# Performance work log

Measured on AMD Instinct MI355X. Metric: run time of the kernel, lower is better.

The kernel has to match this reference:

```python
import jax, jax.numpy as jnp
import numpy as np

DIM = 128
HEADS = 4
WS = 7          # window_size
N = WS * WS     # tokens per window
B_ = 4096       # total windows (64 images x 64 windows)
NW = 64         # windows per image (mask groups)


def _rel_position_index():
    # Matches the torch buffer construction exactly (static, int).
    coords = np.stack(np.meshgrid(np.arange(WS), np.arange(WS), indexing='ij'))
    coords_flat = coords.reshape(2, -1)                      # [2, N]
    rel = coords_flat[:, :, None] - coords_flat[:, None, :]  # [2, N, N]
    rel = rel.transpose(1, 2, 0).copy()                      # [N, N, 2]
    rel[:, :, 0] += WS - 1
    rel[:, :, 1] += WS - 1
    rel[:, :, 0] *= 2 * WS - 1
    return jnp.asarray(rel.sum(-1))                          # [N, N] int


REL_INDEX = _rel_position_index()


def setup_inputs() -> dict:
    key = jax.random.key(0)
    ks = jax.random.split(key, 7)
    x = jax.random.normal(ks[0], (B_, N, DIM), dtype=jnp.float32)
    # shift-style additive mask per window group: mostly 0, some -100
    mask = jnp.where(jax.random.uniform(ks[1], (NW, N, N)) < 0.1, -100.0, 0.0).astype(jnp.float32)
    qkv_w = jax.random.normal(ks[2], (3 * DIM, DIM), dtype=jnp.float32) * (DIM ** -0.5)
    qkv_b = jnp.zeros((3 * DIM,), dtype=jnp.float32)
    proj_w = jax.random.normal(ks[3], (DIM, DIM), dtype=jnp.float32) * (DIM ** -0.5)
    proj_b = jnp.zeros((DIM,), dtype=jnp.float32)
    bias_table = jax.random.normal(ks[4], ((2 * WS - 1) ** 2, HEADS), dtype=jnp.float32) * 0.02
    return {"x": x, "mask": mask, "qkv_w": qkv_w, "qkv_b": qkv_b,
            "proj_w": proj_w, "proj_b": proj_b, "bias_table": bias_table}


def reference(x, mask, qkv_w, qkv_b, proj_w, proj_b, bias_table):
    Bw, Nn, C = x.shape
    H = HEADS
    hd = C // H
    scale = hd ** -0.5
    qkv = (x @ qkv_w.T + qkv_b).reshape(Bw, Nn, 3, H, hd)
    q = jnp.moveaxis(qkv[:, :, 0], 2, 1)  # [B_, H, N, hd]
    k = jnp.moveaxis(qkv[:, :, 1], 2, 1)
    v = jnp.moveaxis(qkv[:, :, 2], 2, 1)
    attn = jnp.einsum('bhnd,bhmd->bhnm', q * scale, k)        # [B_, H, N, N]
    bias = bias_table[REL_INDEX].transpose(2, 0, 1)            # [H, N, N]
    attn = attn + bias[None]
    nW = mask.shape[0]
    attn = attn.reshape(Bw // nW, nW, H, Nn, Nn) + mask[None, :, None]
    attn = attn.reshape(Bw, H, Nn, Nn)
    attn = jax.nn.softmax(attn, axis=-1)
    out = jnp.einsum('bhnm,bhmd->bhnd', attn, v)               # [B_, H, N, hd]
    out = out.transpose(0, 2, 1, 3).reshape(Bw, Nn, C)
    return out @ proj_w.T + proj_b
```

## Files before the change

### kernel.cpp

```cpp
#include <hip/hip_runtime.h>
#include <stdint.h>

typedef float  f32x4   __attribute__((ext_vector_type(4)));
typedef float  float4v __attribute__((ext_vector_type(4)));
typedef short  short4v __attribute__((ext_vector_type(4)));
typedef short  short8v __attribute__((ext_vector_type(8)));
typedef __bf16 bf16x8  __attribute__((ext_vector_type(8)));

static __device__ __forceinline__ short f2bf(float f) {
  unsigned u = __builtin_bit_cast(unsigned, f);
  u += 0x7FFFu + ((u >> 16) & 1u);
  return (short)(u >> 16);
}

static __device__ __forceinline__ f32x4 mfma16(short8v a, short8v b, f32x4 c) {
  return __builtin_amdgcn_mfma_f32_16x16x32_bf16(
      __builtin_bit_cast(bf16x8, a), __builtin_bit_cast(bf16x8, b), c, 0, 0, 0);
}

static __device__ __forceinline__ short8v cat44(short4v a, short4v b) {
  short8v r;
  r[0] = a[0]; r[1] = a[1]; r[2] = a[2]; r[3] = a[3];
  r[4] = b[0]; r[5] = b[1]; r[6] = b[2]; r[7] = b[3];
  return r;
}

__global__ void cvt_weights_kernel(const float* __restrict__ qkv_w,
                                   const float* __restrict__ proj_w,
                                   short* __restrict__ wq, short* __restrict__ wp) {
  int i = blockIdx.x * 256 + threadIdx.x;
  wq[i] = f2bf(qkv_w[i]);
  if (i < 16384) wp[i] = f2bf(proj_w[i]);
}

__global__ void build_cmb_kernel(const float* __restrict__ mask,
                                 const float* __restrict__ bias_table,
                                 float* __restrict__ cmb) {
  int id   = blockIdx.x * 256 + threadIdx.x;
  int lane = id & 63;
  int i    = (id >> 6) & 3;
  int qt   = (id >> 8) & 3;
  int h    = (id >> 10) & 3;
  int w    = id >> 12;
  int q     = qt * 16 + (lane & 15);
  int kbase = i * 16 + ((lane >> 4) << 2);
  f32x4 v;
#pragma unroll
  for (int r = 0; r < 4; ++r) {
    int key = kbase + r;
    float val;
    if (key >= 49) {
      val = -1e30f;
    } else if (q >= 49) {
      val = 0.f;
    } else {
      int qi = q / 7, qj = q - qi * 7;
      int ki = key / 7, kj = key - ki * 7;
      int ridx = (qi - ki + 6) * 13 + (qj - kj + 6);
      val = bias_table[ridx * 4 + h] + mask[w * 2401 + q * 49 + key];
    }
    v[r] = val;
  }
  ((f32x4*)cmb)[id] = v;
}

__global__ __launch_bounds__(256, 2)
void win_attn_kernel(const float* __restrict__ x,
                     const float* __restrict__ qkv_b,
                     const float* __restrict__ proj_b,
                     const short* __restrict__ wq,
                     const short* __restrict__ wp,
                     const float* __restrict__ cmb,
                     float* __restrict__ out) {
  __shared__ __align__(16) short smem[17408];
  short* xb  = smem;
  short* vtm = smem + 8704;
  short* aom = smem;

  const int b    = blockIdx.x;
  const int tid  = threadIdx.x;
  const int lane = tid & 63;
  const int h    = tid >> 6;
  const int l15  = lane & 15;
  const int lhi  = lane >> 4;
  const int cb   = lhi * 8;

  {
    short4v z = {0, 0, 0, 0};
    for (int idx = tid; idx < 510; idx += 256)
      *(short4v*)&xb[49 * 136 + idx * 4] = z;
    const float* xw = x + (long)b * (49 * 128);
    for (int idx = tid; idx < 1568; idx += 256) {
      int m  = idx >> 5;
      int c0 = (idx & 31) << 2;
      float4v v = *(const float4v*)&xw[m * 128 + c0];
      short4v s;
      s[0] = f2bf(v[0]); s[1] = f2bf(v[1]); s[2] = f2bf(v[2]); s[3] = f2bf(v[3]);
      *(short4v*)&xb[m * 136 + c0] = s;
    }
  }
  __syncthreads();

  short8v qfr[4], kfr[4];
  {
    f32x4 qa[2][4], ka[2][4];
#pragma unroll
    for (int nt = 0; nt < 2; ++nt) {
      const f32x4 bq4 = *(const f32x4*)&qkv_b[h * 32 + nt * 16 + lhi * 4];
      const f32x4 bk4 = *(const f32x4*)&qkv_b[128 + h * 32 + nt * 16 + lhi * 4];
#pragma unroll
      for (int jt = 0; jt < 4; ++jt) { qa[nt][jt] = bq4; ka[nt][jt] = bk4; }
    }
#pragma unroll
    for (int ks = 0; ks < 4; ++ks) {
      short8v a[4];
#pragma unroll
      for (int jt = 0; jt < 4; ++jt)
        a[jt] = *(const short8v*)&xb[(jt * 16 + l15) * 136 + ks * 32 + cb];
#pragma unroll
      for (int nt = 0; nt < 2; ++nt) {
        const short8v bq =
            *(const short8v*)&wq[(h * 32 + nt * 16 + l15) * 128 + ks * 32 + cb];
        const short8v bk =
            *(const short8v*)&wq[(128 + h * 32 + nt * 16 + l15) * 128 + ks * 32 + cb];
#pragma unroll
        for (int jt = 0; jt < 4; ++jt) {
          qa[nt][jt] = mfma16(bq, a[jt], qa[nt][jt]);
          ka[nt][jt] = mfma16(bk, a[jt], ka[nt][jt]);
        }
      }
    }
    const float scale = 0.1767766952966369f;
#pragma unroll
    for (int jt = 0; jt < 4; ++jt) {
      short8v qv, kv;
#pragma unroll
      for (int nt = 0; nt < 2; ++nt)
#pragma unroll
        for (int r = 0; r < 4; ++r) {
          qv[nt * 4 + r] = f2bf(qa[nt][jt][r] * scale);
          kv[nt * 4 + r] = f2bf(ka[nt][jt][r]);
        }
      qfr[jt] = qv;
      kfr[jt] = kv;
    }
  }

  {
    f32x4 va[2][4];
#pragma unroll
    for (int nt = 0; nt < 2; ++nt) {
      const float vb = qkv_b[256 + h * 32 + nt * 16 + l15];
#pragma unroll
      for (int mt = 0; mt < 4; ++mt) va[nt][mt] = f32x4{vb, vb, vb, vb};
    }
#pragma unroll
    for (int ks = 0; ks < 4; ++ks) {
      short8v a[4];
#pragma unroll
      for (int mt = 0; mt < 4; ++mt)
        a[mt] = *(const short8v*)&xb[(mt * 16 + l15) * 136 + ks * 32 + cb];
#pragma unroll
      for (int nt = 0; nt < 2; ++nt) {
        const short8v bv =
            *(const short8v*)&wq[(256 + h * 32 + nt * 16 + l15) * 128 + ks * 32 + cb];
#pragma unroll
        for (int mt = 0; mt < 4; ++mt)
          va[nt][mt] = mfma16(a[mt], bv, va[nt][mt]);
      }
    }
#pragma unroll
    for (int nt = 0; nt < 2; ++nt)
#pragma unroll
      for (int mt = 0; mt < 4; ++mt) {
        short4v p;
#pragma unroll
        for (int r = 0; r < 4; ++r) p[r] = f2bf(va[nt][mt][r]);
        *(short4v*)&vtm[h * 2176 + (nt * 16 + l15) * 68 + mt * 16 + lhi * 4] = p;
      }
  }

  f32x4 o[2][4];
#pragma unroll
  for (int dt = 0; dt < 2; ++dt)
#pragma unroll
    for (int jt = 0; jt < 4; ++jt) o[dt][jt] = f32x4{0.f, 0.f, 0.f, 0.f};
  {
    const f32x4* cmb4 = (const f32x4*)cmb;
    const long cbase = (long)(b & 63) * 4096 + h * 1024 + lane;

#pragma unroll
    for (int jt = 0; jt < 4; ++jt) {
      f32x4 s[4];
#pragma unroll
      for (int i = 0; i < 4; ++i)
        s[i] = mfma16(kfr[i], qfr[jt], cmb4[cbase + jt * 256 + i * 64]);

      float mx = s[0][0];
#pragma unroll
      for (int i = 0; i < 4; ++i)
#pragma unroll
        for (int r = 0; r < 4; ++r) mx = fmaxf(mx, s[i][r]);
      mx = fmaxf(mx, __shfl_xor(mx, 16));
      mx = fmaxf(mx, __shfl_xor(mx, 32));
      float sum = 0.f;
#pragma unroll
      for (int i = 0; i < 4; ++i)
#pragma unroll
        for (int r = 0; r < 4; ++r) {
          float e = __expf(s[i][r] - mx);
          s[i][r] = e;
          sum += e;
        }
      sum += __shfl_xor(sum, 16);
      sum += __shfl_xor(sum, 32);
      const float inv = 1.f / sum;

      short8v pb[2];
#pragma unroll
      for (int ks = 0; ks < 2; ++ks) {
        short8v pv;
#pragma unroll
        for (int e = 0; e < 4; ++e) pv[e]     = f2bf(s[2 * ks][e] * inv);
#pragma unroll
        for (int e = 0; e < 4; ++e) pv[4 + e] = f2bf(s[2 * ks + 1][e] * inv);
        pb[ks] = pv;
      }

#pragma unroll
      for (int dt = 0; dt < 2; ++dt)
#pragma unroll
        for (int ks = 0; ks < 2; ++ks) {
          const int va = h * 2176 + (dt * 16 + l15) * 68 + ks * 32 + lhi * 4;
          short8v vfr = cat44(*(const short4v*)&vtm[va], *(const short4v*)&vtm[va + 16]);
          o[dt][jt] = mfma16(vfr, pb[ks], o[dt][jt]);
        }
    }
  }
  __syncthreads();

#pragma unroll
  for (int dt = 0; dt < 2; ++dt)
#pragma unroll
    for (int jt = 0; jt < 4; ++jt) {
      short4v p;
#pragma unroll
      for (int r = 0; r < 4; ++r) p[r] = f2bf(o[dt][jt][r]);
      *(short4v*)&aom[(jt * 16 + l15) * 136 + h * 32 + dt * 16 + lhi * 4] = p;
    }
  __syncthreads();

  {
    f32x4 po[2][4];
#pragma unroll
    for (int nt = 0; nt < 2; ++nt) {
      const float pbv = proj_b[h * 32 + nt * 16 + l15];
#pragma unroll
      for (int mt = 0; mt < 4; ++mt) po[nt][mt] = f32x4{pbv, pbv, pbv, pbv};
    }
#pragma unroll
    for (int ks = 0; ks < 4; ++ks) {
      short8v p[4];
#pragma unroll
      for (int mt = 0; mt < 4; ++mt)
        p[mt] = *(const short8v*)&aom[(mt * 16 + l15) * 136 + ks * 32 + cb];
#pragma unroll
      for (int nt = 0; nt < 2; ++nt) {
        const short8v wfr =
            *(const short8v*)&wp[(h * 32 + nt * 16 + l15) * 128 + ks * 32 + cb];
#pragma unroll
        for (int mt = 0; mt < 4; ++mt)
          po[nt][mt] = mfma16(p[mt], wfr, po[nt][mt]);
      }
    }
    float* outw = out + (long)b * (49 * 128);
#pragma unroll
    for (int nt = 0; nt < 2; ++nt) {
      const int ncol = h * 32 + nt * 16 + l15;
#pragma unroll
      for (int mt = 0; mt < 4; ++mt)
#pragma unroll
        for (int r = 0; r < 4; ++r) {
          const int m0 = mt * 16 + lhi * 4 + r;
          if (m0 < 49) outw[m0 * 128 + ncol] = po[nt][mt][r];
        }
    }
  }
}

extern "C" void kernel_launch(void* const* d_in, const int* in_sizes, int n_in,
                              void* d_out, int out_size, void* d_ws, size_t ws_size,
                              hipStream_t stream) {
  const float* x          = (const float*)d_in[0];
  const float* mask       = (const float*)d_in[1];
  const float* qkv_w      = (const float*)d_in[2];
  const float* qkv_b      = (const float*)d_in[3];
  const float* proj_w     = (const float*)d_in[4];
  const float* proj_b     = (const float*)d_in[5];
  const float* bias_table = (const float*)d_in[6];

  short* wq  = (short*)d_ws;
  short* wp  = wq + 49152;
  float* cmb = (float*)((char*)d_ws + 131072);

  cvt_weights_kernel<<<dim3(192), dim3(256), 0, stream>>>(qkv_w, proj_w, wq, wp);
  build_cmb_kernel<<<dim3(1024), dim3(256), 0, stream>>>(mask, bias_table, cmb);
  win_attn_kernel<<<dim3(4096), dim3(256), 0, stream>>>(
      x, qkv_b, proj_b, wq, wp, cmb, (float*)d_out);
}
```

Baseline: 117.0 us.

## Process eight windows per block with register-prefetched double-buffered input

Each block now loops over 8 consecutive windows instead of handling one, and the grid shrinks from 4096 to 512 blocks. The next window's x tile is loaded into registers during the current window's compute, then converted to bf16 into the alternate LDS buffer. A separate LDS region for the attention output also removes one barrier per window. The aim is to hide global load latency and cut block launch overhead. In exchange LDS per block doubles and the prefetch uses extra registers, which lowers occupancy to about two blocks per CU.

```diff
diff --git a/kernel.cpp b/kernel.cpp
--- a/kernel.cpp
+++ b/kernel.cpp
@@ -72,219 +72,246 @@
                      const short* __restrict__ wp,
                      const float* __restrict__ cmb,
                      float* __restrict__ out) {
-  __shared__ __align__(16) short smem[17408];
-  short* xb  = smem;
-  short* vtm = smem + 8704;
-  short* aom = smem;
-
-  const int b    = blockIdx.x;
+  __shared__ __align__(16) short smem[34816];
+  short* vtm = smem + 17408;
+  short* aom = smem + 26112;
+
   const int tid  = threadIdx.x;
   const int lane = tid & 63;
   const int h    = tid >> 6;
   const int l15  = lane & 15;
   const int lhi  = lane >> 4;
   const int cb   = lhi * 8;
+  const int wbase = blockIdx.x * 8;
+  const float scale = 0.1767766952966369f;
 
   {
     short4v z = {0, 0, 0, 0};
-    for (int idx = tid; idx < 510; idx += 256)
-      *(short4v*)&xb[49 * 136 + idx * 4] = z;
-    const float* xw = x + (long)b * (49 * 128);
-    for (int idx = tid; idx < 1568; idx += 256) {
-      int m  = idx >> 5;
-      int c0 = (idx & 31) << 2;
-      float4v v = *(const float4v*)&xw[m * 128 + c0];
-      short4v s;
-      s[0] = f2bf(v[0]); s[1] = f2bf(v[1]); s[2] = f2bf(v[2]); s[3] = f2bf(v[3]);
-      *(short4v*)&xb[m * 136 + c0] = s;
+    for (int i = tid; i < 510; i += 256) {
+      *(short4v*)&smem[49 * 136 + i * 4]        = z;
+      *(short4v*)&smem[8704 + 49 * 136 + i * 4] = z;
+    }
+    const float* xw = x + (long)wbase * 6272;
+#pragma unroll
+    for (int k = 0; k < 7; ++k) {
+      const int idx = tid + k * 256;
+      if (idx < 1568) {
+        float4v v = *(const float4v*)&xw[idx * 4];
+        short4v s;
+        s[0] = f2bf(v[0]); s[1] = f2bf(v[1]); s[2] = f2bf(v[2]); s[3] = f2bf(v[3]);
+        *(short4v*)&smem[(idx >> 5) * 136 + ((idx & 31) << 2)] = s;
+      }
     }
   }
   __syncthreads();
 
-  short8v qfr[4], kfr[4];
-  {
-    f32x4 qa[2][4], ka[2][4];
-#pragma unroll
-    for (int nt = 0; nt < 2; ++nt) {
-      const f32x4 bq4 = *(const f32x4*)&qkv_b[h * 32 + nt * 16 + lhi * 4];
-      const f32x4 bk4 = *(const f32x4*)&qkv_b[128 + h * 32 + nt * 16 + lhi * 4];
-#pragma unroll
-      for (int jt = 0; jt < 4; ++jt) { qa[nt][jt] = bq4; ka[nt][jt] = bk4; }
-    }
-#pragma unroll
-    for (int ks = 0; ks < 4; ++ks) {
-      short8v a[4];
-#pragma unroll
-      for (int jt = 0; jt < 4; ++jt)
-        a[jt] = *(const short8v*)&xb[(jt * 16 + l15) * 136 + ks * 32 + cb];
+  int cur = 0;
+  for (int wloc = 0; wloc < 8; ++wloc) {
+    const int w = wbase + wloc;
+    const short* xb = smem + cur * 8704;
+
+    float4v pf[7];
+    const bool havenext = (wloc < 7);
+    if (havenext) {
+      const float* xwn = x + (long)(w + 1) * 6272;
+#pragma unroll
+      for (int k = 0; k < 7; ++k) {
+        const int idx = tid + k * 256;
+        if (idx < 1568) pf[k] = *(const float4v*)&xwn[idx * 4];
+      }
+    }
+
+    short8v qfr[4], kfr[4];
+    {
+      f32x4 qa[2][4], ka[2][4];
 #pragma unroll
       for (int nt = 0; nt < 2; ++nt) {
-        const short8v bq =
-            *(const short8v*)&wq[(h * 32 + nt * 16 + l15) * 128 + ks * 32 + cb];
-        const short8v bk =
-            *(const short8v*)&wq[(128 + h * 32 + nt * 16 + l15) * 128 + ks * 32 + cb];
-#pragma unroll
-        for (int jt = 0; jt < 4; ++jt) {
-          qa[nt][jt] = mfma16(bq, a[jt], qa[nt][jt]);
-          ka[nt][jt] = mfma16(bk, a[jt], ka[nt][jt]);
-        }
-      }
-    }
-    const float scale = 0.1767766952966369f;
-#pragma unroll
-    for (int jt = 0; jt < 4; ++jt) {
-      short8v qv, kv;
+        const f32x4 bq4 = *(const f32x4*)&qkv_b[h * 32 + nt * 16 + lhi * 4];
+        const f32x4 bk4 = *(const f32x4*)&qkv_b[128 + h * 32 + nt * 16 + lhi * 4];
+#pragma unroll
+        for (int jt = 0; jt < 4; ++jt) { qa[nt][jt] = bq4; ka[nt][jt] = bk4; }
+      }
+#pragma unroll
+      for (int ks = 0; ks < 4; ++ks) {
+        short8v a[4];
+#pragma unroll
+        for (int jt = 0; jt < 4; ++jt)
+          a[jt] = *(const short8v*)&xb[(jt * 16 + l15) * 136 + ks * 32 + cb];
+#pragma unroll
+        for (int nt = 0; nt < 2; ++nt) {
+          const short8v bq =
+              *(const short8v*)&wq[(h * 32 + nt * 16 + l15) * 128 + ks * 32 + cb];
+          const short8v bk =
+              *(const short8v*)&wq[(128 + h * 32 + nt * 16 + l15) * 128 + ks * 32 + cb];
+#pragma unroll
+          for (int jt = 0; jt < 4; ++jt) {
+            qa[nt][jt] = mfma16(bq, a[jt], qa[nt][jt]);
+            ka[nt][jt] = mfma16(bk, a[jt], ka[nt][jt]);
+          }
+        }
+      }
+#pragma unroll
+      for (int jt = 0; jt < 4; ++jt) {
+        short8v qv, kv;
+#pragma unroll
+        for (int nt = 0; nt < 2; ++nt)
+#pragma unroll
+          for (int r = 0; r < 4; ++r) {
+            qv[nt * 4 + r] = f2bf(qa[nt][jt][r] * scale);
+            kv[nt * 4 + r] = f2bf(ka[nt][jt][r]);
+          }
+        qfr[jt] = qv;
+        kfr[jt] = kv;
+      }
+    }
+
+    {
+      f32x4 va[2][4];
+#pragma unroll
+      for (int nt = 0; nt < 2; ++nt) {
+        const float vb = qkv_b[256 + h * 32 + nt * 16 + l15];
+#pragma unroll
+        for (int mt = 0; mt < 4; ++mt) va[nt][mt] = f32x4{vb, vb, vb, vb};
+      }
+#pragma unroll
+      for (int ks = 0; ks < 4; ++ks) {
+        short8v a[4];
+#pragma unroll
+        for (int mt = 0; mt < 4; ++mt)
+          a[mt] = *(const short8v*)&xb[(mt * 16 + l15) * 136 + ks * 32 + cb];
+#pragma unroll
+        for (int nt = 0; nt < 2; ++nt) {
+          const short8v bv =
+              *(const short8v*)&wq[(256 + h * 32 + nt * 16 + l15) * 128 + ks * 32 + cb];
+#pragma unroll
+          for (int mt = 0; mt < 4; ++mt)
+            va[nt][mt] = mfma16(a[mt], bv, va[nt][mt]);
+        }
+      }
 #pragma unroll
       for (int nt = 0; nt < 2; ++nt)
 #pragma unroll
-        for (int r = 0; r < 4; ++r) {
-          qv[nt * 4 + r] = f2bf(qa[nt][jt][r] * scale);
-          kv[nt * 4 + r] = f2bf(ka[nt][jt][r]);
-        }
-      qfr[jt] = qv;
-      kfr[jt] = kv;
-    }
-  }
-
-  {
-    f32x4 va[2][4];
-#pragma unroll
-    for (int nt = 0; nt < 2; ++nt) {
-      const float vb = qkv_b[256 + h * 32 + nt * 16 + l15];
-#pragma unroll
-      for (int mt = 0; mt < 4; ++mt) va[nt][mt] = f32x4{vb, vb, vb, vb};
-    }
-#pragma unroll
-    for (int ks = 0; ks < 4; ++ks) {
-      short8v a[4];
-#pragma unroll
-      for (int mt = 0; mt < 4; ++mt)
-        a[mt] = *(const short8v*)&xb[(mt * 16 + l15) * 136 + ks * 32 + cb];
+        for (int mt = 0; mt < 4; ++mt) {
+          short4v p;
+#pragma unroll
+          for (int r = 0; r < 4; ++r) p[r] = f2bf(va[nt][mt][r]);
+          *(short4v*)&vtm[h * 2176 + (nt * 16 + l15) * 68 + mt * 16 + lhi * 4] = p;
+        }
+    }
+
+    {
+      const f32x4* cmb4 = (const f32x4*)cmb;
+      const long cbase = (long)(w & 63) * 4096 + h * 1024 + lane;
+
+#pragma unroll
+      for (int jt = 0; jt < 4; ++jt) {
+        f32x4 s[4];
+#pragma unroll
+        for (int i = 0; i < 4; ++i)
+          s[i] = mfma16(kfr[i], qfr[jt], cmb4[cbase + jt * 256 + i * 64]);
+
+        float mx = s[0][0];
+#pragma unroll
+        for (int i = 0; i < 4; ++i)
+#pragma unroll
+          for (int r = 0; r < 4; ++r) mx = fmaxf(mx, s[i][r]);
+        mx = fmaxf(mx, __shfl_xor(mx, 16));
+        mx = fmaxf(mx, __shfl_xor(mx, 32));
+        float sum = 0.f;
+#pragma unroll
+        for (int i = 0; i < 4; ++i)
+#pragma unroll
+          for (int r = 0; r < 4; ++r) {
+            float e = __expf(s[i][r] - mx);
+            s[i][r] = e;
+            sum += e;
+          }
+        sum += __shfl_xor(sum, 16);
+        sum += __shfl_xor(sum, 32);
+        const float inv = 1.f / sum;
+
+        short8v pb[2];
+#pragma unroll
+        for (int ks = 0; ks < 2; ++ks) {
+          short8v pv;
+#pragma unroll
+          for (int e = 0; e < 4; ++e) pv[e]     = f2bf(s[2 * ks][e] * inv);
+#pragma unroll
+          for (int e = 0; e < 4; ++e) pv[4 + e] = f2bf(s[2 * ks + 1][e] * inv);
+          pb[ks] = pv;
+        }
+
+#pragma unroll
+        for (int dt = 0; dt < 2; ++dt) {
+          f32x4 o = {0.f, 0.f, 0.f, 0.f};
+#pragma unroll
+          for (int ks = 0; ks < 2; ++ks) {
+            const int va = h * 2176 + (dt * 16 + l15) * 68 + ks * 32 + lhi * 4;
+            short8v vfr =
+                cat44(*(const short4v*)&vtm[va], *(const short4v*)&vtm[va + 16]);
+            o = mfma16(vfr, pb[ks], o);
+          }
+          short4v p;
+#pragma unroll
+          for (int r = 0; r < 4; ++r) p[r] = f2bf(o[r]);
+          *(short4v*)&aom[(jt * 16 + l15) * 136 + h * 32 + dt * 16 + lhi * 4] = p;
+        }
+      }
+    }
+    __syncthreads();
+
+    {
+      f32x4 po[2][4];
 #pragma unroll
       for (int nt = 0; nt < 2; ++nt) {
-        const short8v bv =
-            *(const short8v*)&wq[(256 + h * 32 + nt * 16 + l15) * 128 + ks * 32 + cb];
+        const float pbv = proj_b[h * 32 + nt * 16 + l15];
+#pragma unroll
+        for (int mt = 0; mt < 4; ++mt) po[nt][mt] = f32x4{pbv, pbv, pbv, pbv};
+      }
+#pragma unroll
+      for (int ks = 0; ks < 4; ++ks) {
+        short8v p[4];
 #pragma unroll
         for (int mt = 0; mt < 4; ++mt)
-          va[nt][mt] = mfma16(a[mt], bv, va[nt][mt]);
-      }
-    }
-#pragma unroll
-    for (int nt = 0; nt < 2; ++nt)
-#pragma unroll
-      for (int mt = 0; mt < 4; ++mt) {
-        short4v p;
-#pragma unroll
-        for (int r = 0; r < 4; ++r) p[r] = f2bf(va[nt][mt][r]);
-        *(short4v*)&vtm[h * 2176 + (nt * 16 + l15) * 68 + mt * 16 + lhi * 4] = p;
-      }
-  }
-
-  f32x4 o[2][4];
-#pragma unroll
-  for (int dt = 0; dt < 2; ++dt)
-#pragma unroll
-    for (int jt = 0; jt < 4; ++jt) o[dt][jt] = f32x4{0.f, 0.f, 0.f, 0.f};
-  {
-    const f32x4* cmb4 = (const f32x4*)cmb;
-    const long cbase = (long)(b & 63) * 4096 + h * 1024 + lane;
-
-#pragma unroll
-    for (int jt = 0; jt < 4; ++jt) {
-      f32x4 s[4];
-#pragma unroll
-      for (int i = 0; i < 4; ++i)
-        s[i] = mfma16(kfr[i], qfr[jt], cmb4[cbase + jt * 256 + i * 64]);
-
-      float mx = s[0][0];
-#pragma unroll
-      for (int i = 0; i < 4; ++i)
-#pragma unroll
-        for (int r = 0; r < 4; ++r) mx = fmaxf(mx, s[i][r]);
-      mx = fmaxf(mx, __shfl_xor(mx, 16));
-      mx = fmaxf(mx, __shfl_xor(mx, 32));
-      float sum = 0.f;
-#pragma unroll
-      for (int i = 0; i < 4; ++i)
-#pragma unroll
-        for (int r = 0; r < 4; ++r) {
-          float e = __expf(s[i][r] - mx);
-          s[i][r] = e;
-          sum += e;
-        }
-      sum += __shfl_xor(sum, 16);
-      sum += __shfl_xor(sum, 32);
-      const float inv = 1.f / sum;
-
-      short8v pb[2];
-#pragma unroll
-      for (int ks = 0; ks < 2; ++ks) {
-        short8v pv;
-#pragma unroll
-        for (int e = 0; e < 4; ++e) pv[e]     = f2bf(s[2 * ks][e] * inv);
-#pragma unroll
-        for (int e = 0; e < 4; ++e) pv[4 + e] = f2bf(s[2 * ks + 1][e] * inv);
-        pb[ks] = pv;
-      }
-
-#pragma unroll
-      for (int dt = 0; dt < 2; ++dt)
-#pragma unroll
-        for (int ks = 0; ks < 2; ++ks) {
-          const int va = h * 2176 + (dt * 16 + l15) * 68 + ks * 32 + lhi * 4;
-          short8v vfr = cat44(*(const short4v*)&vtm[va], *(const short4v*)&vtm[va + 16]);
-          o[dt][jt] = mfma16(vfr, pb[ks], o[dt][jt]);
-        }
-    }
-  }
-  __syncthreads();
-
-#pragma unroll
-  for (int dt = 0; dt < 2; ++dt)
-#pragma unroll
-    for (int jt = 0; jt < 4; ++jt) {
-      short4v p;
-#pragma unroll
-      for (int r = 0; r < 4; ++r) p[r] = f2bf(o[dt][jt][r]);
-      *(short4v*)&aom[(jt * 16 + l15) * 136 + h * 32 + dt * 16 + lhi * 4] = p;
-    }
-  __syncthreads();
-
-  {
-    f32x4 po[2][4];
-#pragma unroll
-    for (int nt = 0; nt < 2; ++nt) {
-      const float pbv = proj_b[h * 32 + nt * 16 + l15];
-#pragma unroll
-      for (int mt = 0; mt < 4; ++mt) po[nt][mt] = f32x4{pbv, pbv, pbv, pbv};
-    }
-#pragma unroll
-    for (int ks = 0; ks < 4; ++ks) {
-      short8v p[4];
-#pragma unroll
-      for (int mt = 0; mt < 4; ++mt)
-        p[mt] = *(const short8v*)&aom[(mt * 16 + l15) * 136 + ks * 32 + cb];
+          p[mt] = *(const short8v*)&aom[(mt * 16 + l15) * 136 + ks * 32 + cb];
+#pragma unroll
+        for (int nt = 0; nt < 2; ++nt) {
+          const short8v wfr =
+              *(const short8v*)&wp[(h * 32 + nt * 16 + l15) * 128 + ks * 32 + cb];
+#pragma unroll
+          for (int mt = 0; mt < 4; ++mt)
+            po[nt][mt] = mfma16(p[mt], wfr, po[nt][mt]);
+        }
+      }
+      float* outw = out + (long)w * 6272;
 #pragma unroll
       for (int nt = 0; nt < 2; ++nt) {
-        const short8v wfr =
-            *(const short8v*)&wp[(h * 32 + nt * 16 + l15) * 128 + ks * 32 + cb];
+        const int ncol = h * 32 + nt * 16 + l15;
 #pragma unroll
         for (int mt = 0; mt < 4; ++mt)
-          po[nt][mt] = mfma16(p[mt], wfr, po[nt][mt]);
-      }
-    }
-    float* outw = out + (long)b * (49 * 128);
-#pragma unroll
-    for (int nt = 0; nt < 2; ++nt) {
-      const int ncol = h * 32 + nt * 16 + l15;
-#pragma unroll
-      for (int mt = 0; mt < 4; ++mt)
-#pragma unroll
-        for (int r = 0; r < 4; ++r) {
-          const int m0 = mt * 16 + lhi * 4 + r;
-          if (m0 < 49) outw[m0 * 128 + ncol] = po[nt][mt][r];
-        }
-    }
+#pragma unroll
+          for (int r = 0; r < 4; ++r) {
+            const int tok = mt * 16 + lhi * 4 + r;
+            if (tok < 49) outw[tok * 128 + ncol] = po[nt][mt][r];
+          }
+      }
+    }
+
+    if (havenext) {
+      short* dst = smem + (cur ^ 1) * 8704;
+#pragma unroll
+      for (int k = 0; k < 7; ++k) {
+        const int idx = tid + k * 256;
+        if (idx < 1568) {
+          short4v s;
+          s[0] = f2bf(pf[k][0]); s[1] = f2bf(pf[k][1]);
+          s[2] = f2bf(pf[k][2]); s[3] = f2bf(pf[k][3]);
+          *(short4v*)&dst[(idx >> 5) * 136 + ((idx & 31) << 2)] = s;
+        }
+      }
+    }
+    __syncthreads();
+    cur ^= 1;
   }
 }
 
@@ -305,6 +332,6 @@
 
   cvt_weights_kernel<<<dim3(192), dim3(256), 0, stream>>>(qkv_w, proj_w, wq, wp);
   build_cmb_kernel<<<dim3(1024), dim3(256), 0, stream>>>(mask, bias_table, cmb);
-  win_attn_kernel<<<dim3(4096), dim3(256), 0, stream>>>(
+  win_attn_kernel<<<dim3(512), dim3(256), 0, stream>>>(
       x, qkv_b, proj_b, wq, wp, cmb, (float*)d_out);
 }
```

New measurement: 261.6 us. 2.24x slower.

## Process two windows per block to reuse weight and bias loads

Applied to the files above, without the earlier changes.

Each block now handles two windows, blockIdx and blockIdx+2048, with separate shared-memory buffers. Every weight fragment and combined bias/mask tile loaded from global memory feeds MFMAs for both windows, which halves those loads and adds independent instruction streams for latency hiding. Because wB equals wA+2048 and 2048 is a multiple of 64, both windows share the same mask group. The cost is double the LDS (about 68KB) and double the accumulator registers, which may cut occupancy below the launch-bounds target of 2 and cause register spills.

```diff
diff --git a/kernel.cpp b/kernel.cpp
--- a/kernel.cpp
+++ b/kernel.cpp
@@ -72,51 +72,67 @@
                      const short* __restrict__ wp,
                      const float* __restrict__ cmb,
                      float* __restrict__ out) {
-  __shared__ __align__(16) short smem[17408];
-  short* xb  = smem;
-  short* vtm = smem + 8704;
-  short* aom = smem;
-
-  const int b    = blockIdx.x;
+  __shared__ __align__(16) short smem[34816];
+  short* xbA  = smem;
+  short* xbB  = smem + 8704;
+  short* vtmA = smem + 17408;
+  short* vtmB = smem + 26112;
+  short* aomA = smem;
+  short* aomB = smem + 8704;
+
   const int tid  = threadIdx.x;
   const int lane = tid & 63;
   const int h    = tid >> 6;
   const int l15  = lane & 15;
   const int lhi  = lane >> 4;
   const int cb   = lhi * 8;
+  const int wA   = blockIdx.x;
+  const int wB   = blockIdx.x + 2048;
+  const float scale = 0.1767766952966369f;
 
   {
     short4v z = {0, 0, 0, 0};
-    for (int idx = tid; idx < 510; idx += 256)
-      *(short4v*)&xb[49 * 136 + idx * 4] = z;
-    const float* xw = x + (long)b * (49 * 128);
+    for (int i = tid; i < 510; i += 256) {
+      *(short4v*)&xbA[49 * 136 + i * 4] = z;
+      *(short4v*)&xbB[49 * 136 + i * 4] = z;
+    }
+    const float* xwA = x + (long)wA * 6272;
+    const float* xwB = x + (long)wB * 6272;
     for (int idx = tid; idx < 1568; idx += 256) {
-      int m  = idx >> 5;
-      int c0 = (idx & 31) << 2;
-      float4v v = *(const float4v*)&xw[m * 128 + c0];
-      short4v s;
-      s[0] = f2bf(v[0]); s[1] = f2bf(v[1]); s[2] = f2bf(v[2]); s[3] = f2bf(v[3]);
-      *(short4v*)&xb[m * 136 + c0] = s;
+      const int m  = idx >> 5;
+      const int c0 = (idx & 31) << 2;
+      float4v vA = *(const float4v*)&xwA[m * 128 + c0];
+      float4v vB = *(const float4v*)&xwB[m * 128 + c0];
+      short4v sA, sB;
+#pragma unroll
+      for (int r = 0; r < 4; ++r) { sA[r] = f2bf(vA[r]); sB[r] = f2bf(vB[r]); }
+      *(short4v*)&xbA[m * 136 + c0] = sA;
+      *(short4v*)&xbB[m * 136 + c0] = sB;
     }
   }
   __syncthreads();
 
-  short8v qfr[4], kfr[4];
-  {
-    f32x4 qa[2][4], ka[2][4];
+  short8v qfrA[4], kfrA[4], qfrB[4], kfrB[4];
+  {
+    f32x4 qaA[2][4], kaA[2][4], qaB[2][4], kaB[2][4];
 #pragma unroll
     for (int nt = 0; nt < 2; ++nt) {
       const f32x4 bq4 = *(const f32x4*)&qkv_b[h * 32 + nt * 16 + lhi * 4];
       const f32x4 bk4 = *(const f32x4*)&qkv_b[128 + h * 32 + nt * 16 + lhi * 4];
 #pragma unroll
-      for (int jt = 0; jt < 4; ++jt) { qa[nt][jt] = bq4; ka[nt][jt] = bk4; }
+      for (int jt = 0; jt < 4; ++jt) {
+        qaA[nt][jt] = bq4; kaA[nt][jt] = bk4;
+        qaB[nt][jt] = bq4; kaB[nt][jt] = bk4;
+      }
     }
 #pragma unroll
     for (int ks = 0; ks < 4; ++ks) {
-      short8v a[4];
-#pragma unroll
-      for (int jt = 0; jt < 4; ++jt)
-        a[jt] = *(const short8v*)&xb[(jt * 16 + l15) * 136 + ks * 32 + cb];
+      short8v aA[4], aB[4];
+#pragma unroll
+      for (int jt = 0; jt < 4; ++jt) {
+        aA[jt] = *(const short8v*)&xbA[(jt * 16 + l15) * 136 + ks * 32 + cb];
+        aB[jt] = *(const short8v*)&xbB[(jt * 16 + l15) * 136 + ks * 32 + cb];
+      }
 #pragma unroll
       for (int nt = 0; nt < 2; ++nt) {
         const short8v bq =
@@ -125,106 +141,139 @@
             *(const short8v*)&wq[(128 + h * 32 + nt * 16 + l15) * 128 + ks * 32 + cb];
 #pragma unroll
         for (int jt = 0; jt < 4; ++jt) {
-          qa[nt][jt] = mfma16(bq, a[jt], qa[nt][jt]);
-          ka[nt][jt] = mfma16(bk, a[jt], ka[nt][jt]);
-        }
-      }
-    }
-    const float scale = 0.1767766952966369f;
+          qaA[nt][jt] = mfma16(bq, aA[jt], qaA[nt][jt]);
+          qaB[nt][jt] = mfma16(bq, aB[jt], qaB[nt][jt]);
+          kaA[nt][jt] = mfma16(bk, aA[jt], kaA[nt][jt]);
+          kaB[nt][jt] = mfma16(bk, aB[jt], kaB[nt][jt]);
+        }
+      }
+    }
 #pragma unroll
     for (int jt = 0; jt < 4; ++jt) {
-      short8v qv, kv;
+      short8v qvA, kvA, qvB, kvB;
 #pragma unroll
       for (int nt = 0; nt < 2; ++nt)
 #pragma unroll
         for (int r = 0; r < 4; ++r) {
-          qv[nt * 4 + r] = f2bf(qa[nt][jt][r] * scale);
-          kv[nt * 4 + r] = f2bf(ka[nt][jt][r]);
-        }
-      qfr[jt] = qv;
-      kfr[jt] = kv;
-    }
-  }
-
-  {
-    f32x4 va[2][4];
+          qvA[nt * 4 + r] = f2bf(qaA[nt][jt][r] * scale);
+          kvA[nt * 4 + r] = f2bf(kaA[nt][jt][r]);
+          qvB[nt * 4 + r] = f2bf(qaB[nt][jt][r] * scale);
+          kvB[nt * 4 + r] = f2bf(kaB[nt][jt][r]);
+        }
+      qfrA[jt] = qvA; kfrA[jt] = kvA;
+      qfrB[jt] = qvB; kfrB[jt] = kvB;
+    }
+  }
+
+  {
+    f32x4 vaA[2][4], vaB[2][4];
 #pragma unroll
     for (int nt = 0; nt < 2; ++nt) {
       const float vb = qkv_b[256 + h * 32 + nt * 16 + l15];
 #pragma unroll
-      for (int mt = 0; mt < 4; ++mt) va[nt][mt] = f32x4{vb, vb, vb, vb};
+      for (int mt = 0; mt < 4; ++mt) {
+        vaA[nt][mt] = f32x4{vb, vb, vb, vb};
+        vaB[nt][mt] = vaA[nt][mt];
+      }
     }
 #pragma unroll
     for (int ks = 0; ks < 4; ++ks) {
-      short8v a[4];
-#pragma unroll
-      for (int mt = 0; mt < 4; ++mt)
-        a[mt] = *(const short8v*)&xb[(mt * 16 + l15) * 136 + ks * 32 + cb];
+      short8v aA[4], aB[4];
+#pragma unroll
+      for (int mt = 0; mt < 4; ++mt) {
+        aA[mt] = *(const short8v*)&xbA[(mt * 16 + l15) * 136 + ks * 32 + cb];
+        aB[mt] = *(const short8v*)&xbB[(mt * 16 + l15) * 136 + ks * 32 + cb];
+      }
 #pragma unroll
       for (int nt = 0; nt < 2; ++nt) {
         const short8v bv =
             *(const short8v*)&wq[(256 + h * 32 + nt * 16 + l15) * 128 + ks * 32 + cb];
 #pragma unroll
-        for (int mt = 0; mt < 4; ++mt)
-          va[nt][mt] = mfma16(a[mt], bv, va[nt][mt]);
+        for (int mt = 0; mt < 4; ++mt) {
+          vaA[nt][mt] = mfma16(aA[mt], bv, vaA[nt][mt]);
+          vaB[nt][mt] = mfma16(aB[mt], bv, vaB[nt][mt]);
+        }
       }
     }
 #pragma unroll
     for (int nt = 0; nt < 2; ++nt)
 #pragma unroll
       for (int mt = 0; mt < 4; ++mt) {
-        short4v p;
-#pragma unroll
-        for (int r = 0; r < 4; ++r) p[r] = f2bf(va[nt][mt][r]);
-        *(short4v*)&vtm[h * 2176 + (nt * 16 + l15) * 68 + mt * 16 + lhi * 4] = p;
-      }
-  }
-
-  f32x4 o[2][4];
+        short4v pA, pB;
+#pragma unroll
+        for (int r = 0; r < 4; ++r) {
+          pA[r] = f2bf(vaA[nt][mt][r]);
+          pB[r] = f2bf(vaB[nt][mt][r]);
+        }
+        *(short4v*)&vtmA[h * 2176 + (nt * 16 + l15) * 68 + mt * 16 + lhi * 4] = pA;
+        *(short4v*)&vtmB[h * 2176 + (nt * 16 + l15) * 68 + mt * 16 + lhi * 4] = pB;
+      }
+  }
+
+  f32x4 oA[2][4], oB[2][4];
 #pragma unroll
   for (int dt = 0; dt < 2; ++dt)
 #pragma unroll
-    for (int jt = 0; jt < 4; ++jt) o[dt][jt] = f32x4{0.f, 0.f, 0.f, 0.f};
+    for (int jt = 0; jt < 4; ++jt) {
+      oA[dt][jt] = f32x4{0.f, 0.f, 0.f, 0.f};
+      oB[dt][jt] = oA[dt][jt];
+    }
   {
     const f32x4* cmb4 = (const f32x4*)cmb;
-    const long cbase = (long)(b & 63) * 4096 + h * 1024 + lane;
+    const long cbase = (long)(wA & 63) * 4096 + h * 1024 + lane;
 
 #pragma unroll
     for (int jt = 0; jt < 4; ++jt) {
-      f32x4 s[4];
+      f32x4 sA[4], sB[4];
+#pragma unroll
+      for (int i = 0; i < 4; ++i) {
+        const f32x4 cv = cmb4[cbase + jt * 256 + i * 64];
+        sA[i] = mfma16(kfrA[i], qfrA[jt], cv);
+        sB[i] = mfma16(kfrB[i], qfrB[jt], cv);
+      }
+
+      float mxA = sA[0][0], mxB = sB[0][0];
 #pragma unroll
       for (int i = 0; i < 4; ++i)
-        s[i] = mfma16(kfr[i], qfr[jt], cmb4[cbase + jt * 256 + i * 64]);
-
-      float mx = s[0][0];
+#pragma unroll
+        for (int r = 0; r < 4; ++r) {
+          mxA = fmaxf(mxA, sA[i][r]);
+          mxB = fmaxf(mxB, sB[i][r]);
+        }
+      mxA = fmaxf(mxA, __shfl_xor(mxA, 16));
+      mxB = fmaxf(mxB, __shfl_xor(mxB, 16));
+      mxA = fmaxf(mxA, __shfl_xor(mxA, 32));
+      mxB = fmaxf(mxB, __shfl_xor(mxB, 32));
+      float sumA = 0.f, sumB = 0.f;
 #pragma unroll
       for (int i = 0; i < 4; ++i)
 #pragma unroll
-        for (int r = 0; r < 4; ++r) mx = fmaxf(mx, s[i][r]);
-      mx = fmaxf(mx, __shfl_xor(mx, 16));
-      mx = fmaxf(mx, __shfl_xor(mx, 32));
-      float sum = 0.f;
-#pragma unroll
-      for (int i = 0; i < 4; ++i)
-#pragma unroll
-        for (int r = 0; r < 4; ++r) {
-          float e = __expf(s[i][r] - mx);
-          s[i][r] = e;
-          sum += e;
-        }
-      sum += __shfl_xor(sum, 16);
-      sum += __shfl_xor(sum, 32);
-      const float inv = 1.f / sum;
-
-      short8v pb[2];
+        for (int r = 0; r < 4; ++r) {
+          float eA = __expf(sA[i][r] - mxA);
+          float eB = __expf(sB[i][r] - mxB);
+          sA[i][r] = eA; sumA += eA;
+          sB[i][r] = eB; sumB += eB;
+        }
+      sumA += __shfl_xor(sumA, 16);
+      sumB += __shfl_xor(sumB, 16);
+      sumA += __shfl_xor(sumA, 32);
+      sumB += __shfl_xor(sumB, 32);
+      const float invA = 1.f / sumA;
+      const float invB = 1.f / sumB;
+
+      short8v pbA[2], pbB[2];
 #pragma unroll
       for (int ks = 0; ks < 2; ++ks) {
-        short8v pv;
-#pragma unroll
-        for (int e = 0; e < 4; ++e) pv[e]     = f2bf(s[2 * ks][e] * inv);
-#pragma unroll
-        for (int e = 0; e < 4; ++e) pv[4 + e] = f2bf(s[2 * ks + 1][e] * inv);
-        pb[ks] = pv;
+        short8v pvA, pvB;
+#pragma unroll
+        for (int e = 0; e < 4; ++e) {
+          pvA[e]     = f2bf(sA[2 * ks][e] * invA);
+          pvA[4 + e] = f2bf(sA[2 * ks + 1][e] * invA);
+          pvB[e]     = f2bf(sB[2 * ks][e] * invB);
+          pvB[4 + e] = f2bf(sB[2 * ks + 1][e] * invB);
+        }
+        pbA[ks] = pvA;
+        pbB[ks] = pvB;
       }
 
 #pragma unroll
@@ -232,8 +281,12 @@
 #pragma unroll
         for (int ks = 0; ks < 2; ++ks) {
           const int va = h * 2176 + (dt * 16 + l15) * 68 + ks * 32 + lhi * 4;
-          short8v vfr = cat44(*(const short4v*)&vtm[va], *(const short4v*)&vtm[va + 16]);
-          o[dt][jt] = mfma16(vfr, pb[ks], o[dt][jt]);
+          short8v vfA = cat44(*(const short4v*)&vtmA[va],
+                              *(const short4v*)&vtmA[va + 16]);
+          short8v vfB = cat44(*(const short4v*)&vtmB[va],
+                              *(const short4v*)&vtmB[va + 16]);
+          oA[dt][jt] = mfma16(vfA, pbA[ks], oA[dt][jt]);
+          oB[dt][jt] = mfma16(vfB, pbB[ks], oB[dt][jt]);
         }
     }
   }
@@ -243,37 +296,49 @@
   for (int dt = 0; dt < 2; ++dt)
 #pragma unroll
     for (int jt = 0; jt < 4; ++jt) {
-      short4v p;
-#pragma unroll
-      for (int r = 0; r < 4; ++r) p[r] = f2bf(o[dt][jt][r]);
-      *(short4v*)&aom[(jt * 16 + l15) * 136 + h * 32 + dt * 16 + lhi * 4] = p;
+      short4v pA, pB;
+#pragma unroll
+      for (int r = 0; r < 4; ++r) {
+        pA[r] = f2bf(oA[dt][jt][r]);
+        pB[r] = f2bf(oB[dt][jt][r]);
+      }
+      *(short4v*)&aomA[(jt * 16 + l15) * 136 + h * 32 + dt * 16 + lhi * 4] = pA;
+      *(short4v*)&aomB[(jt * 16 + l15) * 136 + h * 32 + dt * 16 + lhi * 4] = pB;
     }
   __syncthreads();
 
   {
-    f32x4 po[2][4];
+    f32x4 poA[2][4], poB[2][4];
 #pragma unroll
     for (int nt = 0; nt < 2; ++nt) {
       const float pbv = proj_b[h * 32 + nt * 16 + l15];
 #pragma unroll
-      for (int mt = 0; mt < 4; ++mt) po[nt][mt] = f32x4{pbv, pbv, pbv, pbv};
+      for (int mt = 0; mt < 4; ++mt) {
+        poA[nt][mt] = f32x4{pbv, pbv, pbv, pbv};
+        poB[nt][mt] = poA[nt][mt];
+      }
     }
 #pragma unroll
     for (int ks = 0; ks < 4; ++ks) {
-      short8v p[4];
-#pragma unroll
-      for (int mt = 0; mt < 4; ++mt)
-        p[mt] = *(const short8v*)&aom[(mt * 16 + l15) * 136 + ks * 32 + cb];
+      short8v pA[4], pB[4];
+#pragma unroll
+      for (int mt = 0; mt < 4; ++mt) {
+        pA[mt] = *(const short8v*)&aomA[(mt * 16 + l15) * 136 + ks * 32 + cb];
+        pB[mt] = *(const short8v*)&aomB[(mt * 16 + l15) * 136 + ks * 32 + cb];
+      }
 #pragma unroll
       for (int nt = 0; nt < 2; ++nt) {
         const short8v wfr =
             *(const short8v*)&wp[(h * 32 + nt * 16 + l15) * 128 + ks * 32 + cb];
 #pragma unroll
-        for (int mt = 0; mt < 4; ++mt)
-          po[nt][mt] = mfma16(p[mt], wfr, po[nt][mt]);
-      }
-    }
-    float* outw = out + (long)b * (49 * 128);
+        for (int mt = 0; mt < 4; ++mt) {
+          poA[nt][mt] = mfma16(pA[mt], wfr, poA[nt][mt]);
+          poB[nt][mt] = mfma16(pB[mt], wfr, poB[nt][mt]);
+        }
+      }
+    }
+    float* outA = out + (long)wA * 6272;
+    float* outB = out + (long)wB * 6272;
 #pragma unroll
     for (int nt = 0; nt < 2; ++nt) {
       const int ncol = h * 32 + nt * 16 + l15;
@@ -281,8 +346,11 @@
       for (int mt = 0; mt < 4; ++mt)
 #pragma unroll
         for (int r = 0; r < 4; ++r) {
-          const int m0 = mt * 16 + lhi * 4 + r;
-          if (m0 < 49) outw[m0 * 128 + ncol] = po[nt][mt][r];
+          const int tok = mt * 16 + lhi * 4 + r;
+          if (tok < 49) {
+            outA[tok * 128 + ncol] = poA[nt][mt][r];
+            outB[tok * 128 + ncol] = poB[nt][mt][r];
+          }
         }
     }
   }
@@ -305,6 +373,6 @@
 
   cvt_weights_kernel<<<dim3(192), dim3(256), 0, stream>>>(qkv_w, proj_w, wq, wp);
   build_cmb_kernel<<<dim3(1024), dim3(256), 0, stream>>>(mask, bias_table, cmb);
-  win_attn_kernel<<<dim3(4096), dim3(256), 0, stream>>>(
+  win_attn_kernel<<<dim3(2048), dim3(256), 0, stream>>>(
       x, qkv_b, proj_b, wq, wp, cmb, (float*)d_out);
 }
```

New measurement: 202.6 us. 1.73x slower.
